# Optimization experiments

Hardware: AMD Instinct MI355X
Metric: run time of the kernel (lower is better)

## Reference

```python
import jax, jax.numpy as jnp
import numpy as np

N_DESC = 2
CC_ITERS = 500  # kornia.contrib.connected_components(num_iterations=500)
MIN_PTS = 10


def find_contours(img):
    """Faithful jax port of findContours: pad, kornia connected_components,
    3x3 Laplacian boundary mask, crop. img: [B,1,H,W] binary float32."""
    B, _, H, W = img.shape
    I = jnp.pad(img, ((0, 0), (0, 0), (1, 1), (1, 1)))
    mask = I == 1.0
    # kornia CC: labels initialized to global linear index, propagated by masked 3x3 max-pool
    idx = jnp.arange(B * (H + 2) * (W + 2), dtype=jnp.float32).reshape(B, 1, H + 2, W + 2)
    out0 = jnp.where(mask, idx, 0.0)

    def body(_, o):
        p = jax.lax.reduce_window(o, -jnp.inf, jax.lax.max,
                                  (1, 1, 3, 3), (1, 1, 1, 1), 'SAME')
        return jnp.where(mask, p, 0.0)

    cc = jax.lax.fori_loop(0, CC_ITERS, body, out0)[:, :, 1:-1, 1:-1]
    kern = jnp.array([[1., 1., 1.], [1., -8., 1.], [1., 1., 1.]], dtype=jnp.float32).reshape(1, 1, 3, 3)
    lap = jax.lax.conv_general_dilated(I, kern, (1, 1), 'SAME')
    boundary = (lap < 0).astype(jnp.float32)[:, :, 1:-1, 1:-1]
    return boundary * cc


find_contours = jax.jit(find_contours)


def _sample_stats(cimg, N):
    """Per-image: unique labels (including 0, as in the original), polar-angle
    sort, Fourier descriptor base A_k = sqrt(a^2+b^2)/len with a,b = sums of
    real/imag FFT coefficients / (k*pi). Returns (centers, A) or None."""
    labels = np.unique(cimg)
    if labels.size == 1:
        return None
    centers, As = [], []
    ks = np.arange(1, N + 1, dtype=np.float64)
    for lb in labels:
        pts = np.argwhere(cimg == lb).astype(np.float64)  # (n, 2) row, col
        c = pts.mean(axis=0)
        ang = np.arctan2(pts[:, 1] - c[1], pts[:, 0] - c[0])
        pts = pts[np.argsort(ang, kind='stable')]
        if pts.shape[0] < MIN_PTS:
            continue
        z = pts[:, 0] + 1j * pts[:, 1]
        Fz = np.fft.fft(z)
        a = Fz.real.sum()
        b = Fz.imag.sum()
        A = np.sqrt((a / (ks * np.pi)) ** 2 + (b / (ks * np.pi)) ** 2) / pts.shape[0]
        centers.append(c)
        As.append(A)
    if len(centers) == 0:
        return None
    return np.stack(centers), np.stack(As)


def _compute_S(pred_c, tgt_c, N):
    """S = sum over batch of sum |A_pred[match] - A_gt| (weight-independent part).
    The descriptor is A * 0.5*w^2 + log(1+w^2); the log term cancels in the
    matched absolute difference, so loss = 0.5*w^2 * S exactly."""
    S = 0.0
    for b in range(pred_c.shape[0]):
        sp = _sample_stats(pred_c[b, 0], N)
        st = _sample_stats(tgt_c[b, 0], N)
        if sp is None or st is None:
            continue
        pc, pA = sp
        tc, tA = st
        if tc.shape[0] <= pc.shape[0]:
            d = ((tc[:, None, :] - pc[None, :, :]) ** 2).sum(-1)
            m = d.argmin(axis=1)
            S += np.abs(pA[m] - tA).sum()
        else:
            d = ((pc[:, None, :] - tc[None, :, :]) ** 2).sum(-1)
            m = d.argmin(axis=1)
            S += np.abs(tA[m] - pA).sum()
    return np.float32(S)


def setup_inputs() -> dict:
    key = jax.random.key(0)
    k1, k2, k3 = jax.random.split(key, 3)
    B, H, W = 8, 512, 512
    # low-frequency logits -> realistic building-like blobs after thresholding
    low_p = jax.random.normal(k1, (B, 1, 16, 16), dtype=jnp.float32)
    pred_seg = jax.image.resize(low_p, (B, 1, H, W), method='bilinear') * 4.0
    low_t = jax.random.normal(k2, (B, 1, 16, 16), dtype=jnp.float32)
    target_label = (jax.image.resize(low_t, (B, 1, H, W), method='bilinear') > 0).astype(jnp.float32)
    descriptors_weight = jax.random.uniform(k3, (), dtype=jnp.float32) + 0.5
    return {"pred_seg": pred_seg, "target_label": target_label,
            "descriptors_weight": descriptors_weight}


def reference(pred_seg, target_label, descriptors_weight):
    N = N_DESC
    pred = (jax.nn.sigmoid(pred_seg) > 0.5).astype(jnp.float32)
    tgt = target_label if target_label.ndim == 4 else target_label[:, None]
    pred_contours = np.asarray(find_contours(pred))
    tgt_contours = np.asarray(find_contours(tgt))
    S = _compute_S(pred_contours, tgt_contours, N)
    # descriptor = A * (1/2 * w^2) + log(1 + w^2); log term cancels in |diff|
    return jnp.asarray(S, jnp.float32) * (0.5 * descriptors_weight ** 2)
```

## Files before the change

kernel.cpp:

```cpp
#include <hip/hip_runtime.h>

typedef unsigned int u32;
typedef unsigned long long u64;

#define BN 8
#define NIMG 16
#define NPIMG (512*512)
#define NPIXC (NIMG*NPIMG)
#define PP (514*514)
#define CAP 8192u
#define SLOT0 8192
#define NSLOT 8193
#define NDN (NIMG*NSLOT)
#define TOTR 66977792u
#define MAXL 512
#define PROP_ITERS 500
#define LH 64

#define TILE_W 96
#define TILE_H 64
#define HALO 16
#define CF4 32
#define NSTRIP 8
#define SROWS 12
#define TPC 6
#define TPR 8
#define TPT (TPR*TPC)
#define PROPBLOCKS (NIMG*TPT)

__device__ __forceinline__ u32 hashL(u32 L) { return (L * 2654435761u) >> 19; }
__device__ __forceinline__ u32 hashS(u32 L) { return (L * 2654435761u) >> 26; }

__device__ __forceinline__ u64 encAng(double a) {
  u64 u = (u64)__double_as_longlong(a);
  return (u >> 63) ? ~u : (u | 0x8000000000000000ull);
}

__device__ __forceinline__ float fmax3(float a, float b, float c) {
  return fmaxf(a, fmaxf(b, c));
}

__device__ __forceinline__ float4 horizf4(float4 M, int tx) {
  float Lw = __shfl_up(M.w, 1);
  float Rx = __shfl_down(M.x, 1);
  if (tx == 0) Lw = 0.f;
  if (tx == CF4 - 1) Rx = 0.f;
  float4 hh;
  hh.x = fmax3(Lw, M.x, M.y);
  hh.y = fmax3(M.x, M.y, M.z);
  hh.z = fmax3(M.y, M.z, M.w);
  hh.w = fmax3(M.z, M.w, Rx);
  return hh;
}

__global__ __launch_bounds__(256) void k_prop(const float* __restrict__ src,
                                              float* __restrict__ dst,
                                              const float* __restrict__ pred,
                                              const float* __restrict__ tgt,
                                              u32* __restrict__ flags,
                                              int niter, int sidx) {
  __shared__ float4 hTopS[2][NSTRIP][CF4];
  __shared__ float4 hBotS[2][NSTRIP][CF4];
  __shared__ int s_flag;
  __shared__ int b_ch0;
  __shared__ u32 s_conv;
  const int tid = threadIdx.x;
  const int bx = blockIdx.x;
  const int j = bx >> 3;
  const int img = ((bx & 7) << 1) + (j >= TPT ? 1 : 0);
  const int tt = (j >= TPT) ? (j - TPT) : j;
  const int tyT = tt / TPC, txT = tt % TPC;
  const int tx = tid & 31, sy = tid >> 5;
  const int gr0 = tyT * TILE_H - HALO + sy * SROWS;
  const int gc = txT * TILE_W - HALO + tx * 4;
  const bool gcok = (gc >= 0 && gc < 512);
  const bool writer = (tx >= 4 && tx <= 27 && gc < 512);

  if (sidx > 0) {
    if (tid == 0) s_conv = atomicAdd(&flags[sidx - 1], 0u);
    __syncthreads();
    if (s_conv == 0u) {
      if (writer) {
        const float* ib = src + img * NPIMG;
        float* ob = dst + img * NPIMG;
#pragma unroll
        for (int r = 0; r < SROWS; ++r) {
          int er = sy * SROWS + r;
          if (er >= HALO && er < HALO + TILE_H) {
            float4 v = *(const float4*)(ib + (gr0 + r) * 512 + gc);
            *(float4*)(ob + (gr0 + r) * 512 + gc) = v;
          }
        }
      }
      return;
    }
  }

  float4 cur[SROWS];
  if (sidx == 0) {
    const int f = img >> 3, b = img & 7;
    const float* fb = (f == 0 ? pred : tgt) + b * NPIMG;
#pragma unroll
    for (int r = 0; r < SROWS; ++r) {
      float4 v = make_float4(0.f, 0.f, 0.f, 0.f);
      int gr = gr0 + r;
      if (gcok && gr >= 0 && gr < 512) {
        float4 x = *(const float4*)(fb + gr * 512 + gc);
        float lb = (float)(b * PP + (gr + 1) * 514 + (gc + 1));
        bool mx, my, mz, mw;
        if (f == 0) { mx = x.x > 0.f; my = x.y > 0.f; mz = x.z > 0.f; mw = x.w > 0.f; }
        else        { mx = x.x == 1.f; my = x.y == 1.f; mz = x.z == 1.f; mw = x.w == 1.f; }
        v.x = mx ? lb : 0.f;
        v.y = my ? lb + 1.f : 0.f;
        v.z = mz ? lb + 2.f : 0.f;
        v.w = mw ? lb + 3.f : 0.f;
      }
      cur[r] = v;
    }
  } else {
    const float* ibase = src + img * NPIMG;
#pragma unroll
    for (int r = 0; r < SROWS; ++r) {
      float4 v = make_float4(0.f, 0.f, 0.f, 0.f);
      int gr = gr0 + r;
      if (gcok && gr >= 0 && gr < 512)
        v = *(const float4*)(ibase + gr * 512 + gc);
      cur[r] = v;
    }
  }

  if (tid == 0) b_ch0 = 0;
  bool changed = false;
  for (int itr = 0; itr < niter; ++itr) {
    const int p = itr & 1;
    const bool chk = (p == 1);
    float4 h[SROWS];
#pragma unroll
    for (int r = 0; r < SROWS; ++r) h[r] = horizf4(cur[r], tx);
    hTopS[p][sy][tx] = h[0];
    hBotS[p][sy][tx] = h[SROWS - 1];
    if (chk && tid == 0) s_flag = 0;
    __syncthreads();
    float4 zero = make_float4(0.f, 0.f, 0.f, 0.f);
    float4 hm = (sy > 0) ? hBotS[p][sy - 1][tx] : zero;
    float4 below = (sy < NSTRIP - 1) ? hTopS[p][sy + 1][tx] : zero;
    bool ch0 = false;
#pragma unroll
    for (int r = 0; r < SROWS; ++r) {
      float4 hc = h[r];
      float4 hp = (r == SROWS - 1) ? below : h[r + 1];
      float4 o = cur[r], v;
      v.x = (o.x > 0.f) ? fmax3(hm.x, hc.x, hp.x) : 0.f;
      v.y = (o.y > 0.f) ? fmax3(hm.y, hc.y, hp.y) : 0.f;
      v.z = (o.z > 0.f) ? fmax3(hm.z, hc.z, hp.z) : 0.f;
      v.w = (o.w > 0.f) ? fmax3(hm.w, hc.w, hp.w) : 0.f;
      if (chk)
        changed = changed || (v.x != o.x) || (v.y != o.y) || (v.z != o.z) || (v.w != o.w);
      if (itr == 0)
        ch0 = ch0 || (v.x != o.x) || (v.y != o.y) || (v.z != o.z) || (v.w != o.w);
      cur[r] = v;
      hm = hc;
    }
    if (itr == 0 && ch0) b_ch0 = 1;
    if (chk) {
      if (changed) s_flag = 1;
      __syncthreads();
      if (s_flag == 0) break;
      changed = false;
    }
  }
  if (tid == 0 && b_ch0) atomicOr(&flags[sidx], 1u);

  if (writer) {
    float* obase = dst + img * NPIMG;
#pragma unroll
    for (int r = 0; r < SROWS; ++r) {
      int er = sy * SROWS + r;
      if (er >= HALO && er < HALO + TILE_H)
        *(float4*)(obase + (gr0 + r) * 512 + gc) = cur[r];
    }
  }
}

__global__ __launch_bounds__(256) void k_cimgcount(const float* __restrict__ V,
                                                   float* __restrict__ Cm,
                                                   u32* __restrict__ key, u32* __restrict__ cnt,
                                                   u32* __restrict__ sr, u32* __restrict__ sc) {
  __shared__ u32 hl[LH], hn[LH], hr[LH], hc2[LH];
  __shared__ u32 s_n, s_r, s_c;
  const int tid = threadIdx.x;
  for (int e = tid; e < LH; e += 256) { hl[e] = 0; hn[e] = 0; hr[e] = 0; hc2[e] = 0; }
  if (tid == 0) { s_n = 0; s_r = 0; s_c = 0; }
  __syncthreads();
  int i = blockIdx.x * 256 + tid;
  int img = i >> 18, q = i & (NPIMG - 1);
  int r = q >> 9, c = q & 511;
  const float* base = V + img * NPIMG;
  float v = base[q];
  float out = 0.f;
  if (v > 0.f) {
    bool z = (r == 0) || (r == 511) || (c == 0) || (c == 511);
    if (!z) {
      float mn = base[q - 513];
      mn = fminf(mn, base[q - 512]); mn = fminf(mn, base[q - 511]);
      mn = fminf(mn, base[q - 1]);   mn = fminf(mn, base[q + 1]);
      mn = fminf(mn, base[q + 511]); mn = fminf(mn, base[q + 512]);
      mn = fminf(mn, base[q + 513]);
      z = (mn == 0.f);
    }
    if (z) out = v;
  }
  Cm[i] = out;
  if (out != 0.f) {
    u32 L = (u32)out;
    u32 h = hashS(L);
    bool ins = false;
    for (u32 pr = 0; pr < LH; ++pr) {
      u32 e = (h + pr) & (LH - 1);
      u32 k = atomicCAS(&hl[e], 0u, L);
      if (k == 0u || k == L) {
        atomicAdd(&hn[e], 1u); atomicAdd(&hr[e], (u32)r); atomicAdd(&hc2[e], (u32)c);
        ins = true; break;
      }
    }
    if (!ins) {
      u32 hg = hashL(L), slot = 0xFFFFFFFFu;
      for (u32 pr = 0; pr < CAP; ++pr) {
        u32 k = key[img * CAP + hg];
        if (k == L) { slot = hg; break; }
        if (k == 0u) {
          u32 old = atomicCAS(&key[img * CAP + hg], 0u, L);
          if (old == 0u || old == L) { slot = hg; break; }
        }
        hg = (hg + 1) & (CAP - 1);
      }
      if (slot != 0xFFFFFFFFu) {
        u32 s = (u32)img * NSLOT + slot;
        atomicAdd(&cnt[s], 1u); atomicAdd(&sr[s], (u32)r); atomicAdd(&sc[s], (u32)c);
      }
    }
    atomicAdd(&s_n, 1u); atomicAdd(&s_r, (u32)r); atomicAdd(&s_c, (u32)c);
  }
  __syncthreads();
  int im = (blockIdx.x * 256) >> 18;
  for (int e = tid; e < LH; e += 256) {
    u32 L = hl[e];
    if (L == 0u) continue;
    u32 hg = hashL(L), slot = 0xFFFFFFFFu;
    for (u32 pr = 0; pr < CAP; ++pr) {
      u32 k = key[im * CAP + hg];
      if (k == L) { slot = hg; break; }
      if (k == 0u) {
        u32 old = atomicCAS(&key[im * CAP + hg], 0u, L);
        if (old == 0u || old == L) { slot = hg; break; }
      }
      hg = (hg + 1) & (CAP - 1);
    }
    if (slot != 0xFFFFFFFFu) {
      u32 s = (u32)im * NSLOT + slot;
      atomicAdd(&cnt[s], hn[e]); atomicAdd(&sr[s], hr[e]); atomicAdd(&sc[s], hc2[e]);
    }
  }
  if (tid == 0 && s_n) {
    u32 s = (u32)im * NSLOT + SLOT0;
    atomicAdd(&cnt[s], s_n); atomicAdd(&sr[s], s_r); atomicAdd(&sc[s], s_c);
  }
}

__global__ __launch_bounds__(256) void k_compact(const u32* __restrict__ key,
                                                 const u32* __restrict__ cnt,
                                                 const u32* __restrict__ sr, const u32* __restrict__ sc,
                                                 u32* __restrict__ nlab, u32* __restrict__ labD,
                                                 u32* __restrict__ cntD, u32* __restrict__ srD,
                                                 u32* __restrict__ scD, u32* __restrict__ slotD) {
  int i = blockIdx.x * 256 + threadIdx.x;
  if (i >= NDN) return;
  int img = i / NSLOT, s = i - img * NSLOT;
  u32 L, n, a, b2;
  if (s < (int)CAP) {
    L = key[img * CAP + s];
    if (L == 0u) return;
    n = cnt[img * NSLOT + s];
    a = sr[img * NSLOT + s]; b2 = sc[img * NSLOT + s];
  } else {
    u32 nn = cnt[img * NSLOT + SLOT0];
    n = NPIMG - nn;
    if (n == 0u) return;
    L = 0u;
    a = TOTR - sr[img * NSLOT + SLOT0]; b2 = TOTR - sc[img * NSLOT + SLOT0];
  }
  u32 j = atomicAdd(&nlab[img], 1u);
  if (j < MAXL) {
    labD[img * MAXL + j] = L; cntD[img * MAXL + j] = n;
    srD[img * MAXL + j] = a;  scD[img * MAXL + j] = b2;
    slotD[img * MAXL + j] = (u32)s;
  }
}

__global__ __launch_bounds__(256) void k_angle(const float* __restrict__ Cm,
                                               const u32* __restrict__ key, const u32* __restrict__ cnt,
                                               const u32* __restrict__ sr, const u32* __restrict__ sc,
                                               u64* __restrict__ amin) {
  __shared__ u32 asl[LH];
  __shared__ u64 amn[LH];
  __shared__ u64 wmin[4];
  const int tid = threadIdx.x;
  for (int e = tid; e < LH; e += 256) { asl[e] = 0; amn[e] = ~0ull; }
  __syncthreads();
  int i = blockIdx.x * 256 + tid;
  int img = i >> 18, q = i & (NPIMG - 1);
  int r = q >> 9, c = q & 511;
  float v = Cm[i];
  u64 e0 = ~0ull;
  if (v == 0.f) {
    u32 base = (u32)img * NSLOT + SLOT0;
    u32 n0 = NPIMG - cnt[base];
    double cr = (double)(TOTR - sr[base]) / (double)n0;
    double cc = (double)(TOTR - sc[base]) / (double)n0;
    e0 = encAng(atan2((double)c - cc, (double)r - cr));
  } else {
    u32 L = (u32)v;
    u32 h = hashL(L);
    for (u32 pr = 0; pr < CAP && key[img * CAP + h] != L; ++pr) h = (h + 1) & (CAP - 1);
    u32 s = (u32)img * NSLOT + h;
    u32 n = cnt[s];
    double cr = (double)sr[s] / (double)n;
    double cc = (double)sc[s] / (double)n;
    u64 enc = encAng(atan2((double)c - cc, (double)r - cr));
    u32 kk = h + 1, hh = hashS(kk);
    bool ins = false;
    for (u32 pr = 0; pr < LH; ++pr) {
      u32 e = (hh + pr) & (LH - 1);
      u32 k = atomicCAS(&asl[e], 0u, kk);
      if (k == 0u || k == kk) { atomicMin(&amn[e], enc); ins = true; break; }
    }
    if (!ins) atomicMin(&amin[s], enc);
  }
  for (int o = 32; o > 0; o >>= 1) {
    u64 other = __shfl_xor(e0, o, 64);
    e0 = other < e0 ? other : e0;
  }
  int lane = tid & 63, wid = tid >> 6;
  if (lane == 0) wmin[wid] = e0;
  __syncthreads();
  int im = (blockIdx.x * 256) >> 18;
  if (tid == 0) {
    u64 m = wmin[0];
    for (int k = 1; k < 4; ++k) m = wmin[k] < m ? wmin[k] : m;
    if (m != ~0ull) atomicMin(&amin[(u32)im * NSLOT + SLOT0], m);
  }
  for (int e = tid; e < LH; e += 256)
    if (asl[e]) atomicMin(&amin[(u32)im * NSLOT + (asl[e] - 1)], amn[e]);
}

__global__ __launch_bounds__(256) void k_idx(const float* __restrict__ Cm,
                                             const u32* __restrict__ key, const u32* __restrict__ cnt,
                                             const u32* __restrict__ sr, const u32* __restrict__ sc,
                                             const u64* __restrict__ amin, u32* __restrict__ imin) {
  __shared__ u32 isl[LH];
  __shared__ u32 imn[LH];
  const int tid = threadIdx.x;
  for (int e = tid; e < LH; e += 256) { isl[e] = 0; imn[e] = 0xFFFFFFFFu; }
  __syncthreads();
  int i = blockIdx.x * 256 + tid;
  int img = i >> 18, q = i & (NPIMG - 1);
  int r = q >> 9, c = q & 511;
  float v = Cm[i];
  u32 sl; double cr, cc;
  if (v == 0.f) {
    sl = SLOT0;
    u32 s = (u32)img * NSLOT + SLOT0;
    u32 n0 = NPIMG - cnt[s];
    cr = (double)(TOTR - sr[s]) / (double)n0;
    cc = (double)(TOTR - sc[s]) / (double)n0;
  } else {
    u32 L = (u32)v;
    u32 h = hashL(L);
    for (u32 pr = 0; pr < CAP && key[img * CAP + h] != L; ++pr) h = (h + 1) & (CAP - 1);
    sl = h;
    u32 s = (u32)img * NSLOT + h;
    u32 n = cnt[s];
    cr = (double)sr[s] / (double)n;
    cc = (double)sc[s] / (double)n;
  }
  u64 e = encAng(atan2((double)c - cc, (double)r - cr));
  if (e == amin[(u32)img * NSLOT + sl]) {
    u32 kk = sl + 1, hh = hashS(kk);
    bool ins = false;
    for (u32 pr = 0; pr < LH; ++pr) {
      u32 e2 = (hh + pr) & (LH - 1);
      u32 k = atomicCAS(&isl[e2], 0u, kk);
      if (k == 0u || k == kk) { atomicMin(&imn[e2], (u32)q); ins = true; break; }
    }
    if (!ins) atomicMin(&imin[(u32)img * NSLOT + sl], (u32)q);
  }
  __syncthreads();
  int im = (blockIdx.x * 256) >> 18;
  for (int e2 = tid; e2 < LH; e2 += 256)
    if (isl[e2]) atomicMin(&imin[(u32)im * NSLOT + (isl[e2] - 1)], imn[e2]);
}

__global__ __launch_bounds__(256) void k_match(const u32* __restrict__ nlab,
                                               const u32* __restrict__ labD, const u32* __restrict__ cntD,
                                               const u32* __restrict__ srD, const u32* __restrict__ scD,
                                               const u32* __restrict__ slotD, const u32* __restrict__ imin,
                                               const float* __restrict__ wp, float* __restrict__ out) {
  __shared__ u32 lbl[2][MAXL];
  __shared__ double cx[2][MAXL], cy[2][MAXL], Rr[2][MAXL];
  __shared__ int nlist[2];
  __shared__ double wsum[4];
  const int tid = threadIdx.x;
  double S = 0.0;
  for (int b = 0; b < BN; ++b) {
    __syncthreads();
    if (tid == 0) { nlist[0] = nlist[1] = 0; }
    __syncthreads();
    int tot[2];
    for (int f = 0; f < 2; ++f) {
      int t = f * BN + b;
      int ntot = (int)nlab[t];
      tot[f] = ntot;
      int nl = ntot > MAXL ? MAXL : ntot;
      for (int s2 = tid; s2 < nl; s2 += 256) {
        u32 n = cntD[t * MAXL + s2];
        if (n < 10u) continue;
        int j = atomicAdd(&nlist[f], 1);
        lbl[f][j] = labD[t * MAXL + s2];
        cx[f][j] = (double)srD[t * MAXL + s2] / (double)n;
        cy[f][j] = (double)scD[t * MAXL + s2] / (double)n;
        u32 pi = imin[t * NSLOT + slotD[t * MAXL + s2]];
        double r0 = (double)(pi >> 9), c0 = (double)(pi & 511u);
        Rr[f][j] = sqrt(r0 * r0 + c0 * c0);
      }
    }
    __syncthreads();
    int np = nlist[0], nt = nlist[1];
    bool valid = (tot[0] >= 2) && (np >= 1) && (tot[1] >= 2) && (nt >= 1);
    if (valid) {
      u32 ml[2][2]; double mx[2][2], my[2][2], mr[2][2]; int rk[2][2]; int nh[2];
      for (int f = 0; f < 2; ++f) {
        int n = f ? nt : np;
        nh[f] = 0;
        for (int i = tid; i < n; i += 256) {
          int k = nh[f]++;
          u32 L = lbl[f][i];
          ml[f][k] = L; mx[f][k] = cx[f][i]; my[f][k] = cy[f][i]; mr[f][k] = Rr[f][i];
          int rr = 0;
          for (int j = 0; j < n; ++j) rr += (lbl[f][j] < L) ? 1 : 0;
          rk[f][k] = rr;
        }
      }
      __syncthreads();
      for (int f = 0; f < 2; ++f)
        for (int k = 0; k < nh[f]; ++k) {
          int rr = rk[f][k];
          lbl[f][rr] = ml[f][k]; cx[f][rr] = mx[f][k];
          cy[f][rr] = my[f][k];  Rr[f][rr] = mr[f][k];
        }
      __syncthreads();
      if (nt <= np) {
        for (int j = tid; j < nt; j += 256) {
          int m = 0; double bd = 1e300;
          double tx0 = cx[1][j], ty0 = cy[1][j];
          for (int i2 = 0; i2 < np; ++i2) {
            double dx = tx0 - cx[0][i2], dy = ty0 - cy[0][i2];
            double d = dx * dx + dy * dy;
            if (d < bd) { bd = d; m = i2; }
          }
          S += fabs(Rr[0][m] - Rr[1][j]);
        }
      } else {
        for (int i2 = tid; i2 < np; i2 += 256) {
          int m = 0; double bd = 1e300;
          double px0 = cx[0][i2], py0 = cy[0][i2];
          for (int j = 0; j < nt; ++j) {
            double dx = px0 - cx[1][j], dy = py0 - cy[1][j];
            double d = dx * dx + dy * dy;
            if (d < bd) { bd = d; m = j; }
          }
          S += fabs(Rr[1][m] - Rr[0][i2]);
        }
      }
    }
  }
  for (int o = 32; o > 0; o >>= 1) S += __shfl_xor(S, o, 64);
  int lane = tid & 63, wid = tid >> 6;
  if (lane == 0) wsum[wid] = S;
  __syncthreads();
  if (tid == 0) {
    double total = wsum[0] + wsum[1] + wsum[2] + wsum[3];
    total *= (1.5 / 3.14159265358979323846);
    float w = wp[0];
    out[0] = (float)total * (0.5f * w * w);
  }
}

extern "C" void kernel_launch(void* const* d_in, const int* in_sizes, int n_in,
                              void* d_out, int out_size, void* d_ws, size_t ws_size,
                              hipStream_t stream) {
  const float* pred = (const float*)d_in[0];
  const float* tgt  = (const float*)d_in[1];
  const float* wp   = (const float*)d_in[2];
  float* out = (float*)d_out;

  char* ws = (char*)d_ws;
  size_t off = 0;
  float* A  = (float*)(ws + off); off += (size_t)NPIXC * 4;
  float* Bb = (float*)(ws + off); off += (size_t)NPIXC * 4;
  u32* key  = (u32*)(ws + off);   off += (size_t)NIMG * CAP * 4;
  u32* cnt  = (u32*)(ws + off);   off += (size_t)NIMG * NSLOT * 4;
  u32* sr   = (u32*)(ws + off);   off += (size_t)NIMG * NSLOT * 4;
  u32* sc   = (u32*)(ws + off);   off += (size_t)NIMG * NSLOT * 4;
  u64* amin = (u64*)(ws + off);   off += (size_t)NIMG * NSLOT * 8;
  u32* imin = (u32*)(ws + off);   off += (size_t)NIMG * NSLOT * 4;
  u32* nlab = (u32*)(ws + off);   off += (size_t)NIMG * 4;
  u32* flags= (u32*)(ws + off);   off += (size_t)64 * 4;
  u32* labD = (u32*)(ws + off);   off += (size_t)NIMG * MAXL * 4;
  u32* cntD = (u32*)(ws + off);   off += (size_t)NIMG * MAXL * 4;
  u32* srD  = (u32*)(ws + off);   off += (size_t)NIMG * MAXL * 4;
  u32* scD  = (u32*)(ws + off);   off += (size_t)NIMG * MAXL * 4;
  u32* slotD= (u32*)(ws + off);   off += (size_t)NIMG * MAXL * 4;

  size_t zlen = (size_t)NIMG * CAP * 4 + 3ull * NIMG * NSLOT * 4;
  hipMemsetAsync(key, 0, zlen, stream);
  hipMemsetAsync(amin, 0xFF, (size_t)NIMG * NSLOT * 12, stream);
  hipMemsetAsync(nlab, 0, (size_t)NIMG * 4 + 64 * 4, stream);

  const int gC = NPIXC / 256;
  const int gS = (NDN + 255) / 256;

  k_prop<<<PROPBLOCKS, 256, 0, stream>>>(A, A, pred, tgt, flags, HALO, 0);
  float* src = A; float* dst = Bb;
  int done = HALO, sidx = 1;
  while (done < PROP_ITERS) {
    int k = PROP_ITERS - done; if (k > HALO) k = HALO;
    k_prop<<<PROPBLOCKS, 256, 0, stream>>>(src, dst, pred, tgt, flags, k, sidx);
    float* t2 = src; src = dst; dst = t2;
    done += k; ++sidx;
  }
  float* Cm = dst;
  k_cimgcount<<<gC, 256, 0, stream>>>(src, Cm, key, cnt, sr, sc);
  k_compact<<<gS, 256, 0, stream>>>(key, cnt, sr, sc, nlab, labD, cntD, srD, scD, slotD);
  k_angle<<<gC, 256, 0, stream>>>(Cm, key, cnt, sr, sc, amin);
  k_idx<<<gC, 256, 0, stream>>>(Cm, key, cnt, sr, sc, amin, imin);
  k_match<<<1, 256, 0, stream>>>(nlab, labD, cntD, srD, scD, slotD, imin, wp, out);
}
```

Measured before the change: 1.580 ms.

## Track per-tile convergence with neighbor bitmasks to skip stable tiles

Replaces the single per-launch global convergence flag with a per-image 64-bit bitmask of tiles whose interior changed, rotated across three buffers. Each launch checks whether any of its 3x3 neighboring tiles changed in the previous launch and, if none did, only copies its tile through. The goal is to skip propagation for tiles that are already stable while others are still converging. The cost is an extra reread of the source tile at the end of each launch to detect interior changes, plus some atomic traffic.

```diff
diff --git a/kernel.cpp b/kernel.cpp
--- a/kernel.cpp
+++ b/kernel.cpp
@@ -53,17 +53,35 @@
   return hh;
 }
 
+__device__ __forceinline__ float4 initVal(const float* __restrict__ pred,
+                                          const float* __restrict__ tgt,
+                                          int img, int gr, int gc) {
+  const int f = img >> 3, b = img & 7;
+  const float* fb = (f == 0 ? pred : tgt) + b * NPIMG;
+  float4 x = *(const float4*)(fb + gr * 512 + gc);
+  float lb = (float)(b * PP + (gr + 1) * 514 + (gc + 1));
+  bool mx, my, mz, mw;
+  if (f == 0) { mx = x.x > 0.f; my = x.y > 0.f; mz = x.z > 0.f; mw = x.w > 0.f; }
+  else        { mx = x.x == 1.f; my = x.y == 1.f; mz = x.z == 1.f; mw = x.w == 1.f; }
+  float4 v;
+  v.x = mx ? lb : 0.f;
+  v.y = my ? lb + 1.f : 0.f;
+  v.z = mz ? lb + 2.f : 0.f;
+  v.w = mw ? lb + 3.f : 0.f;
+  return v;
+}
+
 __global__ __launch_bounds__(256) void k_prop(const float* __restrict__ src,
                                               float* __restrict__ dst,
                                               const float* __restrict__ pred,
                                               const float* __restrict__ tgt,
-                                              u32* __restrict__ flags,
+                                              u64* __restrict__ cmask,
                                               int niter, int sidx) {
   __shared__ float4 hTopS[2][NSTRIP][CF4];
   __shared__ float4 hBotS[2][NSTRIP][CF4];
   __shared__ int s_flag;
-  __shared__ int b_ch0;
-  __shared__ u32 s_conv;
+  __shared__ int b_inner;
+  __shared__ u64 s_m;
   const int tid = threadIdx.x;
   const int bx = blockIdx.x;
   const int j = bx >> 3;
@@ -75,11 +93,22 @@
   const int gc = txT * TILE_W - HALO + tx * 4;
   const bool gcok = (gc >= 0 && gc < 512);
   const bool writer = (tx >= 4 && tx <= 27 && gc < 512);
-
+  const int Wn = sidx % 3, Rn = (sidx + 2) % 3, Cn = (sidx + 1) % 3;
+
+  if (tid == 0) {
+    if (sidx > 0) s_m = atomicAdd(&cmask[Rn * NIMG + img], 0ull);
+    atomicExch(&cmask[Cn * NIMG + img], 0ull);
+  }
+  __syncthreads();
   if (sidx > 0) {
-    if (tid == 0) s_conv = atomicAdd(&flags[sidx - 1], 0u);
-    __syncthreads();
-    if (s_conv == 0u) {
+    u64 nb = 0;
+    for (int dy = -1; dy <= 1; ++dy)
+      for (int dx = -1; dx <= 1; ++dx) {
+        int ny = tyT + dy, nx2 = txT + dx;
+        if (ny >= 0 && ny < TPR && nx2 >= 0 && nx2 < TPC)
+          nb |= 1ull << (ny * TPC + nx2);
+      }
+    if ((s_m & nb) == 0ull) {
       if (writer) {
         const float* ib = src + img * NPIMG;
         float* ob = dst + img * NPIMG;
@@ -98,23 +127,12 @@
 
   float4 cur[SROWS];
   if (sidx == 0) {
-    const int f = img >> 3, b = img & 7;
-    const float* fb = (f == 0 ? pred : tgt) + b * NPIMG;
 #pragma unroll
     for (int r = 0; r < SROWS; ++r) {
       float4 v = make_float4(0.f, 0.f, 0.f, 0.f);
       int gr = gr0 + r;
-      if (gcok && gr >= 0 && gr < 512) {
-        float4 x = *(const float4*)(fb + gr * 512 + gc);
-        float lb = (float)(b * PP + (gr + 1) * 514 + (gc + 1));
-        bool mx, my, mz, mw;
-        if (f == 0) { mx = x.x > 0.f; my = x.y > 0.f; mz = x.z > 0.f; mw = x.w > 0.f; }
-        else        { mx = x.x == 1.f; my = x.y == 1.f; mz = x.z == 1.f; mw = x.w == 1.f; }
-        v.x = mx ? lb : 0.f;
-        v.y = my ? lb + 1.f : 0.f;
-        v.z = mz ? lb + 2.f : 0.f;
-        v.w = mw ? lb + 3.f : 0.f;
-      }
+      if (gcok && gr >= 0 && gr < 512)
+        v = initVal(pred, tgt, img, gr, gc);
       cur[r] = v;
     }
   } else {
@@ -129,7 +147,7 @@
     }
   }
 
-  if (tid == 0) b_ch0 = 0;
+  if (tid == 0) b_inner = 0;
   bool changed = false;
   for (int itr = 0; itr < niter; ++itr) {
     const int p = itr & 1;
@@ -144,7 +162,6 @@
     float4 zero = make_float4(0.f, 0.f, 0.f, 0.f);
     float4 hm = (sy > 0) ? hBotS[p][sy - 1][tx] : zero;
     float4 below = (sy < NSTRIP - 1) ? hTopS[p][sy + 1][tx] : zero;
-    bool ch0 = false;
 #pragma unroll
     for (int r = 0; r < SROWS; ++r) {
       float4 hc = h[r];
@@ -156,12 +173,9 @@
       v.w = (o.w > 0.f) ? fmax3(hm.w, hc.w, hp.w) : 0.f;
       if (chk)
         changed = changed || (v.x != o.x) || (v.y != o.y) || (v.z != o.z) || (v.w != o.w);
-      if (itr == 0)
-        ch0 = ch0 || (v.x != o.x) || (v.y != o.y) || (v.z != o.z) || (v.w != o.w);
       cur[r] = v;
       hm = hc;
     }
-    if (itr == 0 && ch0) b_ch0 = 1;
     if (chk) {
       if (changed) s_flag = 1;
       __syncthreads();
@@ -169,7 +183,26 @@
       changed = false;
     }
   }
-  if (tid == 0 && b_ch0) atomicOr(&flags[sidx], 1u);
+
+  bool innerChanged = false;
+  if (writer) {
+    const float* ib = src + img * NPIMG;
+#pragma unroll
+    for (int r = 0; r < SROWS; ++r) {
+      int er = sy * SROWS + r;
+      if (er >= HALO && er < HALO + TILE_H) {
+        float4 o = (sidx == 0) ? initVal(pred, tgt, img, gr0 + r, gc)
+                               : *(const float4*)(ib + (gr0 + r) * 512 + gc);
+        float4 v = cur[r];
+        innerChanged = innerChanged || (v.x != o.x) || (v.y != o.y) ||
+                       (v.z != o.z) || (v.w != o.w);
+      }
+    }
+  }
+  if (innerChanged) b_inner = 1;
+  __syncthreads();
+  if (tid == 0 && b_inner)
+    atomicOr(&cmask[Wn * NIMG + img], 1ull << tt);
 
   if (writer) {
     float* obase = dst + img * NPIMG;
@@ -514,7 +547,7 @@
   u64* amin = (u64*)(ws + off);   off += (size_t)NIMG * NSLOT * 8;
   u32* imin = (u32*)(ws + off);   off += (size_t)NIMG * NSLOT * 4;
   u32* nlab = (u32*)(ws + off);   off += (size_t)NIMG * 4;
-  u32* flags= (u32*)(ws + off);   off += (size_t)64 * 4;
+  u64* cmask= (u64*)(ws + off);   off += (size_t)3 * NIMG * 8;
   u32* labD = (u32*)(ws + off);   off += (size_t)NIMG * MAXL * 4;
   u32* cntD = (u32*)(ws + off);   off += (size_t)NIMG * MAXL * 4;
   u32* srD  = (u32*)(ws + off);   off += (size_t)NIMG * MAXL * 4;
@@ -524,17 +557,17 @@
   size_t zlen = (size_t)NIMG * CAP * 4 + 3ull * NIMG * NSLOT * 4;
   hipMemsetAsync(key, 0, zlen, stream);
   hipMemsetAsync(amin, 0xFF, (size_t)NIMG * NSLOT * 12, stream);
-  hipMemsetAsync(nlab, 0, (size_t)NIMG * 4 + 64 * 4, stream);
+  hipMemsetAsync(nlab, 0, (size_t)NIMG * 4 + 3 * NIMG * 8, stream);
 
   const int gC = NPIXC / 256;
   const int gS = (NDN + 255) / 256;
 
-  k_prop<<<PROPBLOCKS, 256, 0, stream>>>(A, A, pred, tgt, flags, HALO, 0);
+  k_prop<<<PROPBLOCKS, 256, 0, stream>>>(A, A, pred, tgt, cmask, HALO, 0);
   float* src = A; float* dst = Bb;
   int done = HALO, sidx = 1;
   while (done < PROP_ITERS) {
     int k = PROP_ITERS - done; if (k > HALO) k = HALO;
-    k_prop<<<PROPBLOCKS, 256, 0, stream>>>(src, dst, pred, tgt, flags, k, sidx);
+    k_prop<<<PROPBLOCKS, 256, 0, stream>>>(src, dst, pred, tgt, cmask, k, sidx);
     float* t2 = src; src = dst; dst = t2;
     done += k; ++sidx;
   }
```

Result: slower. 1.725 ms (+9.2%).
